# Performance work log

Hardware: AMD Instinct MI355X
Metric: run time of the kernel (lower is better)

## Reference

```python
import jax, jax.numpy as jnp
import numpy as np

N_FILTERS = 64
FILTER_SIZE = 64
N_FRAMES = 64
N_TO_KEEP = 128
MIN_SIZE = 512
N_SAMPLES = 32768
BATCH = 8


def pos_encoding(n_elements, n_sinusoids):
    t = np.linspace(1e-8, 1.0, n_elements)
    freq = np.linspace(1e-3, 1.0, n_sinusoids)
    return np.sin(t[:, None] * freq[None, :]).astype(np.float32)


def gammatone_filter_bank(n_filters, size, sr=22050.0):
    # 4th-order gammatone impulse responses, linearly spaced center freqs
    t = np.arange(size) / sr
    freqs = np.linspace(20.0, sr / 2 - 20.0, n_filters)
    b = 1.019 * 24.7 * (4.37 * freqs / 1000.0 + 1.0)  # ERB bandwidths
    g = (t[None, :] ** 3) * np.exp(-2 * np.pi * b[:, None] * t[None, :]) \
        * np.cos(2 * np.pi * freqs[:, None] * t[None, :])
    g = g / (np.abs(g).max(axis=-1, keepdims=True) + 1e-12)
    return g.astype(np.float32)


def setup_inputs() -> dict:
    key = jax.random.key(0)
    k1, k2 = jax.random.split(key)
    return {
        'target': jax.random.normal(k1, (BATCH, 1, N_SAMPLES), dtype=jnp.float32),
        'recon': jax.random.normal(k2, (BATCH, 1, N_SAMPLES), dtype=jnp.float32),
        'filters': jnp.asarray(gammatone_filter_bank(N_FILTERS, FILTER_SIZE)),
        'proj_time': jnp.asarray(pos_encoding(N_FRAMES, 128)),
        'proj_freq': jnp.asarray(pos_encoding(N_FILTERS, 128)),
    }


def fft_frequency_decompose(x, min_size):
    # band-limited octave decomposition: band of size s holds rfft bins [s/4, s/2)
    coeffs = jnp.fft.rfft(x, norm='ortho')
    n = x.shape[-1]
    bands = []
    start, end = 0, min_size // 2
    while end <= n // 2:
        spec = jnp.zeros(x.shape[:-1] + (end + 1,), dtype=coeffs.dtype)
        spec = spec.at[..., start:end].set(coeffs[..., start:end])
        bands.append(jnp.fft.irfft(spec, n=end * 2, norm='ortho'))
        start, end = end, end * 2
    return bands


def fft_convolve(a, b):
    n = a.shape[-1]
    pa = jnp.pad(a, [(0, 0)] * (a.ndim - 1) + [(0, n)])
    pb = jnp.pad(b, [(0, 0)] * (b.ndim - 1) + [(0, n)])
    spec = jnp.fft.rfft(pa) * jnp.fft.rfft(pb)  # broadcasts [B,1,.] x [1,F,.]
    return jnp.fft.irfft(spec, n=2 * n)[..., :n]


def max_pool1d(x, kernel, stride, pad):
    return jax.lax.reduce_window(
        x, -jnp.inf, jax.lax.max,
        (1, 1, kernel), (1, 1, stride),
        [(0, 0), (0, 0), (pad, pad)])


def sparsify2(x, k):
    # top-k over flattened (channels*time); pack events as value-scaled time
    # one-hots and binary channel one-hots
    b, c, t = x.shape
    flat = x.reshape(b, c * t)
    values, indices = jax.lax.top_k(flat, k)  # [b, k]
    ch, tm = indices // t, indices % t
    packed = (tm[..., None] == jnp.arange(t)[None, None, :]).astype(x.dtype) * values[..., None]  # [b,k,t]
    one_hot = (ch[..., None] == jnp.arange(c)[None, None, :]).astype(x.dtype)  # [b,k,c]
    return packed, one_hot


def _feature(x, filters, proj_time, proj_freq):
    bands = fft_frequency_decompose(x, MIN_SIZE)
    outs = []
    for band in bands:  # fixed small set of structurally distinct bands
        samples = band.shape[-1]
        filt = jnp.pad(filters[None, :, :], ((0, 0), (0, 0), (0, samples - FILTER_SIZE)))
        result = fft_convolve(band, filt)  # [B, n_filters, samples]
        stride = samples // 64
        pooled = max_pool1d(result, 2 * stride, stride, stride // 2)[..., :samples]  # [B, 64, 64]
        packed, one_hot = sparsify2(pooled, N_TO_KEEP)
        a = packed @ proj_time   # [B, k, 128]
        b = one_hot @ proj_freq  # [B, k, 128]
        outs.append(jnp.concatenate([a, b], axis=-1))
    return jnp.concatenate(outs, axis=-1)  # [B, k, 256 * n_bands]


def reference(target, recon, filters, proj_time, proj_freq):
    t = _feature(target, filters, proj_time, proj_freq)
    r = _feature(recon, filters, proj_time, proj_freq)
    return jnp.abs(t - r).mean()
```

## Files before the change

kernel.cpp:

```cpp
#include <hip/hip_runtime.h>
#include <hip/hip_bf16.h>

#define N_SAMP    32768
#define NBINS     16384
#define NSIG      16
#define NBANDS    7
#define K_TOP     128
#define BAND_STRIDE 65472

#define SST_F   0
#define SST_PT  4096
#define SST_PF  12288
#define SST_TOT 20480

#define TWO_PI 6.283185307179586f

typedef __attribute__((ext_vector_type(8))) short bf16x8;
typedef __attribute__((ext_vector_type(4))) float f32x4;

__device__ __forceinline__ float bf2f(__hip_bfloat16 v) { return __bfloat162float(v); }

__device__ __forceinline__ unsigned encf(float f) {
    unsigned u = __float_as_uint(f);
    return (u & 0x80000000u) ? ~u : (u | 0x80000000u);
}
__device__ __forceinline__ float decf(unsigned u) {
    return __uint_as_float((u & 0x80000000u) ? (u ^ 0x80000000u) : ~u);
}

__device__ __forceinline__ int band_M1sh(int b) { return b < 3 ? 4 : (b < 4 ? 5 : 6); }
__device__ __forceinline__ int band_Lsh(int b) {
    return b == 0 ? 5 : (b == 1 ? 6 : (b < 5 ? 7 : (b == 5 ? 8 : 9)));
}
__device__ __forceinline__ int band_M2sh(int b) {
    return b < 2 ? 4 : (b < 5 ? 5 : (b == 5 ? 6 : 7));
}

__global__ __launch_bounds__(256) void k_fwd1(
    const void* __restrict__ tgt, const void* __restrict__ rec,
    const void* __restrict__ f, const void* __restrict__ pt,
    const void* __restrict__ pf,
    __hip_bfloat16* __restrict__ staged,
    float* __restrict__ bands, float* __restrict__ accum,
    int* __restrict__ counter, int* __restrict__ lossCnt,
    float* __restrict__ T)
{
    const int tid   = threadIdx.x;
    const int sig   = blockIdx.y;

    if (blockIdx.x == 16) {
        float pv0 = bf2f(((const __hip_bfloat16*)tgt)[tid & 63]);
        int bad0 = (fabsf(pv0) > 1e8f) || (pv0 != pv0);
        const int isf = (__ballot(bad0) != 0ull);
        #pragma unroll
        for (int k = 0; k < 5; ++k) {
            int id = sig * 1280 + k * 256 + tid;
            const void* src; int idx;
            if (id < SST_PT)      { src = f;  idx = id; }
            else if (id < SST_PF) { src = pt; idx = id - SST_PT; }
            else                  { src = pf; idx = id - SST_PF; }
            float v = isf ? ((const float*)src)[idx]
                          : bf2f(((const __hip_bfloat16*)src)[idx]);
            staged[id] = __float2bfloat16(v);
        }
        for (int i = tid; i < 448; i += 256) {
            int g = i >> 6, j = i & 63;
            int off = 64 * g + 512 * ((1 << g) - 1);
            bands[(size_t)sig * BAND_STRIDE + off + j] = 0.f;
        }
        if (sig == 0) {
            if (tid == 0) { accum[0] = 0.f; counter[0] = 0; }
            if (tid < 8 * NBANDS) lossCnt[tid] = 0;
        }
        return;
    }

    const int nbase = (blockIdx.x & 1) * 128;
    const int kgrp  = ((blockIdx.x >> 1) & 1) * 64;
    const int nqq   = (blockIdx.x >> 2) & 3;
    __shared__ __align__(16) __hip_bfloat16 xT[32][136];
    __shared__ float ct[128], st[128];
    __shared__ float2 t256[256];
    __shared__ float2 tF[128];

    {
        float sv, cv;
        sincosf(TWO_PI * (float)tid * (1.f / 256.f), &sv, &cv);
        t256[tid] = make_float2(cv, -sv);
        if (tid < 128) {
            sincosf(TWO_PI * (float)tid * (1.f / 128.f), &sv, &cv);
            ct[tid] = cv; st[tid] = sv;
            sincosf(TWO_PI * (float)tid * (1.f / 32768.f), &sv, &cv);
            tF[tid] = make_float2(cv, -sv);
        }
    }

    float pv = bf2f(((const __hip_bfloat16*)tgt)[tid & 63]);
    int bad = (fabsf(pv) > 1e8f) || (pv != pv);
    const int isf32 = (__ballot(bad) != 0ull);
    const void* xsrc = (sig < 8) ? tgt : rec;
    const int soff = (sig & 7) * N_SAMP;

    const int rloc = tid & 31;
    const int chb  = (tid >> 5) * 16;
    for (int c8 = 0; c8 < 16; c8 += 8) {
        union { bf16x8 v; __hip_bfloat16 h[8]; } u;
        #pragma unroll
        for (int uu = 0; uu < 8; ++uu) {
            int n1 = chb + c8 + uu;
            int gi = soff + n1 * 256 + nbase + nqq * 32 + rloc;
            float xv = isf32 ? ((const float*)xsrc)[gi]
                             : bf2f(((const __hip_bfloat16*)xsrc)[gi]);
            u.h[uu] = __float2bfloat16(xv);
        }
        *(bf16x8*)(&xT[rloc][chb + c8]) = u.v;
    }
    __syncthreads();

    const int tl = tid & 15, quad = (tid >> 4) & 3, w = tid >> 6;
    const int k1 = kgrp + w * 16 + tl;
    bf16x8 Arh[4], Arl[4], Aih[4], Ail[4];
    #pragma unroll
    for (int ki = 0; ki < 4; ++ki) {
        union { bf16x8 v; __hip_bfloat16 h[8]; } rh, rl, ih, il;
        #pragma unroll
        for (int j = 0; j < 8; ++j) {
            int n1 = ki * 32 + quad * 8 + j;
            int tt = (k1 * n1) & 127;
            float wre = ct[tt], wim = -st[tt];
            __hip_bfloat16 h1 = __float2bfloat16(wre);
            rh.h[j] = h1;
            rl.h[j] = __float2bfloat16(wre - bf2f(h1));
            __hip_bfloat16 h2 = __float2bfloat16(wim);
            ih.h[j] = h2;
            il.h[j] = __float2bfloat16(wim - bf2f(h2));
        }
        Arh[ki] = rh.v; Arl[ki] = rl.v; Aih[ki] = ih.v; Ail[ki] = il.v;
    }

    float2* To = (float2*)T + (size_t)sig * 128 * 256;
    const int mk = kgrp + w * 16 + quad * 4;
    for (int ni = 0; ni < 2; ++ni) {
        bf16x8 B[4];
        #pragma unroll
        for (int ki = 0; ki < 4; ++ki)
            B[ki] = *(const bf16x8*)(&xT[ni * 16 + tl][ki * 32 + quad * 8]);
        f32x4 aR = {0.f,0.f,0.f,0.f}, aI = {0.f,0.f,0.f,0.f};
        #pragma unroll
        for (int ki = 0; ki < 4; ++ki) {
            aR = __builtin_amdgcn_mfma_f32_16x16x32_bf16(Arh[ki], B[ki], aR, 0, 0, 0);
            aR = __builtin_amdgcn_mfma_f32_16x16x32_bf16(Arl[ki], B[ki], aR, 0, 0, 0);
            aI = __builtin_amdgcn_mfma_f32_16x16x32_bf16(Aih[ki], B[ki], aI, 0, 0, 0);
            aI = __builtin_amdgcn_mfma_f32_16x16x32_bf16(Ail[ki], B[ki], aI, 0, 0, 0);
        }
        const int n2 = nbase + nqq * 32 + ni * 16 + tl;
        #pragma unroll
        for (int rg = 0; rg < 4; ++rg) {
            int k1e = mk + rg;
            int m = k1e * n2;
            float2 e1 = t256[m >> 7];
            float2 e2 = tF[m & 127];
            float er = e1.x * e2.x - e1.y * e2.y;
            float ei = e1.x * e2.y + e1.y * e2.x;
            float Tr = aR[rg] * er - aI[rg] * ei;
            float Ti = aI[rg] * er + aR[rg] * ei;
            To[(size_t)k1e * 256 + n2] = make_float2(Tr, Ti);
        }
    }
}

__global__ __launch_bounds__(128) void k_fwd2(
    const float* __restrict__ T, float* __restrict__ C)
{
    const int k2  = threadIdx.x;
    const int k1  = blockIdx.x;
    const int sig = blockIdx.y;
    __shared__ float2 Ts[256];
    __shared__ float2 tw[256];
    const float2* Tin = (const float2*)T + ((size_t)sig * 128 + k1) * 256;
    for (int i = k2; i < 256; i += 128) Ts[i] = Tin[i];
    {
        float sv, cv;
        sincosf(TWO_PI * (float)k2 * (1.f / 256.f), &sv, &cv);
        tw[k2]       = make_float2(cv, -sv);
        tw[k2 + 128] = make_float2(-cv, sv);
    }
    __syncthreads();
    float er[4], ei[4];
    #pragma unroll
    for (int c = 0; c < 4; ++c) {
        float2 e = tw[(c * k2) & 255];
        er[c] = e.x; ei[c] = e.y;
    }
    float2 e4 = tw[(4 * k2) & 255];
    const float c4 = e4.x, s4 = e4.y;
    float Xr[4] = {0.f,0.f,0.f,0.f}, Xi[4] = {0.f,0.f,0.f,0.f};
    for (int n2 = 0; n2 < 256; n2 += 4) {
        #pragma unroll
        for (int c = 0; c < 4; ++c) {
            float2 t = Ts[n2 + c];
            Xr[c] += t.x * er[c] - t.y * ei[c];
            Xi[c] += t.x * ei[c] + t.y * er[c];
            float nr = er[c] * c4 - ei[c] * s4;
            ei[c]    = er[c] * s4 + ei[c] * c4;
            er[c] = nr;
        }
    }
    const float inv = 5.5242717280199030e-3f;
    float xr = (Xr[0] + Xr[1]) + (Xr[2] + Xr[3]);
    float xi = (Xi[0] + Xi[1]) + (Xi[2] + Xi[3]);
    float2* Co = (float2*)C + (size_t)sig * NBINS;
    Co[k1 + 128 * k2] = make_float2(xr * inv, xi * inv);
}

__global__ __launch_bounds__(256) void k_synthA(
    const float* __restrict__ C, float* __restrict__ G)
{
    const int tid = threadIdx.x;
    const int sig = blockIdx.y;
    const int bix = 63 - blockIdx.x;
    const int band = (bix == 0) ? 0 : (32 - __clz(bix));
    const int lbx  = (band == 0) ? 0 : (bix - (1 << (band - 1)));
    const int s    = 512 << band;
    const int m1sh = band_M1sh(band);
    const int lsh  = band_Lsh(band);
    const int m2sh = band_M2sh(band);
    const int M2   = 1 << m2sh;
    const int L    = 1 << lsh;
    const int L4   = L >> 2;
    const int a    = (band == 0) ? 0 : (128 << band);
    const int tix  = lbx * 256 + tid;
    const int j1lo = (lbx * 256) >> (lsh - 2);
    int j1cnt = 256 >> (lsh - 2);
    if (j1cnt > (1 << m1sh)) j1cnt = 1 << m1sh;
    __shared__ float2 Ds[256];
    const float2* D = (const float2*)C + (size_t)sig * NBINS + a;
    for (int i = tid; i < (j1cnt << m2sh); i += 256) {
        int j1o = i >> m2sh, j2 = i & (M2 - 1);
        Ds[i] = D[(j1lo + j1o) + (j2 << m1sh)];
    }
    __syncthreads();
    if (tix >= (128 << band)) return;
    const int j1o = (tix >> (lsh - 2)) - j1lo;
    const int m   = tix & (L4 - 1);
    const float2* Dj = Ds + (j1o << m2sh);
    float e0r = 1.f, e0i = 0.f, e1r, e1i, sr, si;
    sincosf(TWO_PI * (float)m / (float)L, &e1i, &e1r);
    sr = e1r * e1r - e1i * e1i;
    si = 2.f * e1r * e1i;
    float ar[4] = {0.f,0.f,0.f,0.f}, ai[4] = {0.f,0.f,0.f,0.f};
    for (int j2 = 0; j2 < M2; j2 += 4) {
        {   float2 d = Dj[j2];
            float tr = d.x * e0r - d.y * e0i, ti = d.x * e0i + d.y * e0r;
            ar[0] += tr; ai[0] += ti; ar[1] += tr; ai[1] += ti;
            ar[2] += tr; ai[2] += ti; ar[3] += tr; ai[3] += ti;
            float nr = e0r * sr - e0i * si; e0i = e0r * si + e0i * sr; e0r = nr;
        }
        {   float2 d = Dj[j2 + 1];
            float tr = d.x * e1r - d.y * e1i, ti = d.x * e1i + d.y * e1r;
            ar[0] += tr; ai[0] += ti;
            ar[1] -= ti; ai[1] += tr;
            ar[2] -= tr; ai[2] -= ti;
            ar[3] += ti; ai[3] -= tr;
            float nr = e1r * sr - e1i * si; e1i = e1r * si + e1i * sr; e1r = nr;
        }
        {   float2 d = Dj[j2 + 2];
            float tr = d.x * e0r - d.y * e0i, ti = d.x * e0i + d.y * e0r;
            ar[0] += tr; ai[0] += ti;
            ar[1] -= tr; ai[1] -= ti;
            ar[2] += tr; ai[2] += ti;
            ar[3] -= tr; ai[3] -= ti;
            float nr = e0r * sr - e0i * si; e0i = e0r * si + e0i * sr; e0r = nr;
        }
        {   float2 d = Dj[j2 + 3];
            float tr = d.x * e1r - d.y * e1i, ti = d.x * e1i + d.y * e1r;
            ar[0] += tr; ai[0] += ti;
            ar[1] += ti; ai[1] -= tr;
            ar[2] -= tr; ai[2] -= ti;
            ar[3] -= ti; ai[3] += tr;
            float nr = e1r * sr - e1i * si; e1i = e1r * si + e1i * sr; e1r = nr;
        }
    }
    const float sc = 2.f * rsqrtf((float)s);
    float2* Go = (float2*)G + (size_t)sig * 65024 + 512 * ((1 << band) - 1);
    const int base = ((tix >> (lsh - 2)) << lsh) + m;
    #pragma unroll
    for (int q = 0; q < 4; ++q)
        Go[base + q * L4] = make_float2(ar[q] * sc, ai[q] * sc);
}

__global__ __launch_bounds__(256) void k_synthB(
    const float* __restrict__ C, const float* __restrict__ G,
    float* __restrict__ bands)
{
    const int tid = threadIdx.x;
    const int sig = blockIdx.y;
    const int bix = 63 - blockIdx.x;
    const int band = (bix == 0) ? 0 : (32 - __clz(bix));
    const int lbx  = (band == 0) ? 0 : (bix - (1 << (band - 1)));
    const int s    = 512 << band;
    const int M1   = 1 << band_M1sh(band);
    const int lsh  = band_Lsh(band);
    const int n    = lbx * 256 + tid;
    const int s4   = s >> 2;
    if (n >= s4) return;
    const int m    = n & ((1 << lsh) - 1);
    const float2* Gi = (const float2*)G + (size_t)sig * 65024 + 512 * ((1 << band) - 1);
    float e0r = 1.f, e0i = 0.f, e1r, e1i, sr, si;
    sincosf(TWO_PI * (float)n / (float)s, &e1i, &e1r);
    sr = e1r * e1r - e1i * e1i;
    si = 2.f * e1r * e1i;
    float zr[4] = {0.f,0.f,0.f,0.f}, zi[4] = {0.f,0.f,0.f,0.f};
    for (int j1 = 0; j1 < M1; j1 += 4) {
        {   float2 g = Gi[((j1 + 0) << lsh) + m];
            float tr = g.x * e0r - g.y * e0i, ti = g.x * e0i + g.y * e0r;
            zr[0] += tr; zi[0] += ti; zr[1] += tr; zi[1] += ti;
            zr[2] += tr; zi[2] += ti; zr[3] += tr; zi[3] += ti;
            float nr = e0r * sr - e0i * si; e0i = e0r * si + e0i * sr; e0r = nr;
        }
        {   float2 g = Gi[((j1 + 1) << lsh) + m];
            float tr = g.x * e1r - g.y * e1i, ti = g.x * e1i + g.y * e1r;
            zr[0] += tr; zi[0] += ti;
            zr[1] -= ti; zi[1] += tr;
            zr[2] -= tr; zi[2] -= ti;
            zr[3] += ti; zi[3] -= tr;
            float nr = e1r * sr - e1i * si; e1i = e1r * si + e1i * sr; e1r = nr;
        }
        {   float2 g = Gi[((j1 + 2) << lsh) + m];
            float tr = g.x * e0r - g.y * e0i, ti = g.x * e0i + g.y * e0r;
            zr[0] += tr; zi[0] += ti;
            zr[1] -= tr; zi[1] -= ti;
            zr[2] += tr; zi[2] += ti;
            zr[3] -= tr; zi[3] -= ti;
            float nr = e0r * sr - e0i * si; e0i = e0r * si + e0i * sr; e0r = nr;
        }
        {   float2 g = Gi[((j1 + 3) << lsh) + m];
            float tr = g.x * e1r - g.y * e1i, ti = g.x * e1i + g.y * e1r;
            zr[0] += tr; zi[0] += ti;
            zr[1] += ti; zi[1] -= tr;
            zr[2] -= tr; zi[2] -= ti;
            zr[3] -= ti; zi[3] += tr;
            float nr = e1r * sr - e1i * si; e1i = e1r * si + e1i * sr; e1r = nr;
        }
    }
    const int poff = 64 * (band + 1) + 512 * ((1 << band) - 1);
    float* bo = bands + (size_t)sig * BAND_STRIDE + poff;
    if (band == 0) {
        const float dc = C[(size_t)sig * NBINS * 2] * 0.04419417382415922f;
        #pragma unroll
        for (int q = 0; q < 4; ++q) bo[n + q * s4] = zr[q] - dc;
    } else {
        #pragma unroll
        for (int q = 0; q < 4; ++q) {
            float val;
            switch (n & 3) {
                case 0:  val =  zr[q]; break;
                case 1:  val = -zi[q]; break;
                case 2:  val = -zr[q]; break;
                default: val =  zi[q]; break;
            }
            bo[n + q * s4] = val;
        }
    }
}

__global__ __launch_bounds__(256) void k_conv(
    const float* __restrict__ bands,
    const __hip_bfloat16* __restrict__ filters,
    float* __restrict__ segG)
{
    const int tid  = threadIdx.x;
    const int sig  = blockIdx.y;
    const int c    = blockIdx.x;
    const int band = 31 - __clz(c + 1);
    const int cidx = c + 1 - (1 << band);
    const int poff = 64 * (band + 1) + 512 * ((1 << band) - 1);
    const float* bp = bands + (size_t)sig * BAND_STRIDE + poff + cidx * 512;

    __shared__ __align__(16) __hip_bfloat16 xr[8][584];
    __shared__ float segP[64 * 4];

    if (tid < 72) {
        const int j = tid;
        const float* src = bp + 496 - 8 * j;
        float4 f0 = *(const float4*)(src + 12);
        float4 f1 = *(const float4*)(src + 8);
        float4 f2 = *(const float4*)(src + 4);
        float4 f3 = *(const float4*)(src + 0);
        __hip_bfloat16 w[16];
        w[0]  = __float2bfloat16(f0.w); w[1]  = __float2bfloat16(f0.z);
        w[2]  = __float2bfloat16(f0.y); w[3]  = __float2bfloat16(f0.x);
        w[4]  = __float2bfloat16(f1.w); w[5]  = __float2bfloat16(f1.z);
        w[6]  = __float2bfloat16(f1.y); w[7]  = __float2bfloat16(f1.x);
        w[8]  = __float2bfloat16(f2.w); w[9]  = __float2bfloat16(f2.z);
        w[10] = __float2bfloat16(f2.y); w[11] = __float2bfloat16(f2.x);
        w[12] = __float2bfloat16(f3.w); w[13] = __float2bfloat16(f3.z);
        w[14] = __float2bfloat16(f3.y); w[15] = __float2bfloat16(f3.x);
        #pragma unroll
        for (int p = 0; p < 8; ++p) {
            union { bf16x8 v; __hip_bfloat16 h[8]; } o;
            #pragma unroll
            for (int e = 0; e < 8; ++e) o.h[e] = w[p + e];
            *(bf16x8*)(&xr[p][8 * j]) = o.v;
        }
    }
    __syncthreads();

    const int tl   = tid & 15;
    const int quad = (tid >> 4) & 3;
    const int wave = tid >> 6;

    bf16x8 bf0[4], bf1[4];
    #pragma unroll
    for (int ft = 0; ft < 4; ++ft) {
        const __hip_bfloat16* fp = filters + ((ft * 16 + tl) * 64 + quad * 8);
        bf0[ft] = *(const bf16x8*)(fp);
        bf1[ft] = *(const bf16x8*)(fp + 32);
    }

    int s0 = 511 - wave * 128 - tl + 8 * quad;
    const __hip_bfloat16* xp = &xr[0][0] + (s0 & 7) * 584 + (s0 & ~7);

    const int spc = 512 >> (2 + band);
    float* segO = segG + (size_t)(sig * NBANDS + band) * 64 * 128 + cidx * spc;

    const float NEG = -3.4e38f;
    float run0 = NEG, run1 = NEG, run2 = NEG, run3 = NEG;
    const int per = (band >= 2) ? (1 << (band - 2)) : 1;

    for (int it = 0; it < 8; ++it) {
        const int t0 = wave * 128 + it * 16;
        bf16x8 a0 = *(const bf16x8*)(xp);
        bf16x8 a1 = *(const bf16x8*)(xp + 32);
        xp -= 16;
        f32x4 ac0 = {0.f,0.f,0.f,0.f}, ac1 = ac0, ac2 = ac0, ac3 = ac0;
        ac0 = __builtin_amdgcn_mfma_f32_16x16x32_bf16(a0, bf0[0], ac0, 0, 0, 0);
        ac0 = __builtin_amdgcn_mfma_f32_16x16x32_bf16(a1, bf1[0], ac0, 0, 0, 0);
        ac1 = __builtin_amdgcn_mfma_f32_16x16x32_bf16(a0, bf0[1], ac1, 0, 0, 0);
        ac1 = __builtin_amdgcn_mfma_f32_16x16x32_bf16(a1, bf1[1], ac1, 0, 0, 0);
        ac2 = __builtin_amdgcn_mfma_f32_16x16x32_bf16(a0, bf0[2], ac2, 0, 0, 0);
        ac2 = __builtin_amdgcn_mfma_f32_16x16x32_bf16(a1, bf1[2], ac2, 0, 0, 0);
        ac3 = __builtin_amdgcn_mfma_f32_16x16x32_bf16(a0, bf0[3], ac3, 0, 0, 0);
        ac3 = __builtin_amdgcn_mfma_f32_16x16x32_bf16(a1, bf1[3], ac3, 0, 0, 0);
        float m0 = fmaxf(fmaxf(ac0[0], ac0[1]), fmaxf(ac0[2], ac0[3]));
        float m1 = fmaxf(fmaxf(ac1[0], ac1[1]), fmaxf(ac1[2], ac1[3]));
        float m2 = fmaxf(fmaxf(ac2[0], ac2[1]), fmaxf(ac2[2], ac2[3]));
        float m3 = fmaxf(fmaxf(ac3[0], ac3[1]), fmaxf(ac3[2], ac3[3]));
        if (band == 0) {
            int sb = (t0 >> 2) + quad;
            segO[(tl     ) * 128 + sb] = m0;
            segO[(tl + 16) * 128 + sb] = m1;
            segO[(tl + 32) * 128 + sb] = m2;
            segO[(tl + 48) * 128 + sb] = m3;
        } else if (band == 1) {
            m0 = fmaxf(m0, __shfl_xor(m0, 16));
            m1 = fmaxf(m1, __shfl_xor(m1, 16));
            m2 = fmaxf(m2, __shfl_xor(m2, 16));
            m3 = fmaxf(m3, __shfl_xor(m3, 16));
            if ((quad & 1) == 0) {
                int sb = (t0 >> 3) + (quad >> 1);
                segO[(tl     ) * 128 + sb] = m0;
                segO[(tl + 16) * 128 + sb] = m1;
                segO[(tl + 32) * 128 + sb] = m2;
                segO[(tl + 48) * 128 + sb] = m3;
            }
        } else {
            m0 = fmaxf(m0, __shfl_xor(m0, 16)); m0 = fmaxf(m0, __shfl_xor(m0, 32));
            m1 = fmaxf(m1, __shfl_xor(m1, 16)); m1 = fmaxf(m1, __shfl_xor(m1, 32));
            m2 = fmaxf(m2, __shfl_xor(m2, 16)); m2 = fmaxf(m2, __shfl_xor(m2, 32));
            m3 = fmaxf(m3, __shfl_xor(m3, 16)); m3 = fmaxf(m3, __shfl_xor(m3, 32));
            run0 = fmaxf(run0, m0); run1 = fmaxf(run1, m1);
            run2 = fmaxf(run2, m2); run3 = fmaxf(run3, m3);
            if (((it + 1) & (per - 1)) == 0) {
                int sb = t0 >> (2 + band);
                float rv = quad == 0 ? run0 : quad == 1 ? run1
                         : quad == 2 ? run2 : run3;
                segO[(tl + 16 * quad) * 128 + sb] = rv;
                run0 = NEG; run1 = NEG; run2 = NEG; run3 = NEG;
            }
        }
    }
    if (band == 6) {
        float rv = quad == 0 ? run0 : quad == 1 ? run1
                 : quad == 2 ? run2 : run3;
        segP[(tl + 16 * quad) * 4 + wave] = rv;
        __syncthreads();
        if (tid < 128) {
            int f = tid & 63, sg = tid >> 6;
            segO[f * 128 + sg] =
                fmaxf(segP[f * 4 + 2 * sg], segP[f * 4 + 2 * sg + 1]);
        }
    }
}

__global__ __launch_bounds__(512) void k_topk(
    const float* __restrict__ segG,
    float* __restrict__ topv, int* __restrict__ topi,
    const __hip_bfloat16* __restrict__ PT, const __hip_bfloat16* __restrict__ PF,
    int* __restrict__ lossCnt, float* __restrict__ accum,
    int* __restrict__ counter, unsigned* __restrict__ out)
{
    const int tid = threadIdx.x;
    const int band = blockIdx.x, sig = blockIdx.y;
    const float* segB = segG + (size_t)(sig * NBANDS + band) * 64 * 128;

    __shared__ unsigned hist[256];
    __shared__ unsigned scan[256];
    __shared__ unsigned long long list[512];
    __shared__ int sh_B, sh_nA, sh_cnt, sh_num, sh_w2;
    __shared__ float vT[128], vR[128];
    __shared__ int   iT[128], iR[128];
    __shared__ float red[256];
    __shared__ int amLast;

    unsigned long long kk[8];
    #pragma unroll
    for (int q = 0; q < 8; ++q) {
        int i = q * 512 + tid;
        int f = i >> 6, t = i & 63;
        const float* sg = segB + f * 128;
        float m = fmaxf(sg[2 * t], sg[2 * t + 1]);
        if (t > 0)  m = fmaxf(m, sg[2 * t - 1]);
        if (t < 63) m = fmaxf(m, sg[2 * t + 2]);
        kk[q] = ((unsigned long long)encf(m) << 32) | (unsigned)(4095 - i);
    }

    int shift = 56;
    unsigned long long prefix = 0;
    int nA = 0;
    for (int lev = 0; lev < 8; ++lev) {
        if (tid < 256) hist[tid] = 0;
        __syncthreads();
        #pragma unroll
        for (int q = 0; q < 8; ++q) {
            bool inpre = (lev == 0) || ((kk[q] >> (shift + 8)) == prefix);
            if (inpre) atomicAdd(&hist[(unsigned)((kk[q] >> shift) & 255u)], 1u);
        }
        __syncthreads();
        if (tid < 256) scan[tid] = hist[tid];
        __syncthreads();
        for (int off = 1; off < 256; off <<= 1) {
            unsigned v = 0;
            if (tid < 256) v = scan[tid] + ((tid + off < 256) ? scan[tid + off] : 0u);
            __syncthreads();
            if (tid < 256) scan[tid] = v;
            __syncthreads();
        }
        if (tid < 256) {
            unsigned ge = (unsigned)nA + scan[tid];
            unsigned gt = (unsigned)nA + ((tid < 255) ? scan[tid + 1] : 0u);
            if (ge >= 128u && gt < 128u) {
                sh_B = tid; sh_nA = (int)gt; sh_cnt = (int)hist[tid];
            }
        }
        __syncthreads();
        prefix = (prefix << 8) | (unsigned)sh_B;
        nA = sh_nA;
        if (nA + sh_cnt <= 511 || shift == 0) break;
        shift -= 8;
        __syncthreads();
    }

    if (tid < 256) { list[tid] = 0ull; list[tid + 256] = 0ull; }
    if (tid == 0) sh_num = 0;
    __syncthreads();
    #pragma unroll
    for (int q = 0; q < 8; ++q) {
        if ((kk[q] >> shift) >= prefix) {
            int p = atomicAdd(&sh_num, 1);
            if (p < 512) list[p] = kk[q];
        }
    }
    __syncthreads();

    for (int k = 2; k <= 512; k <<= 1) {
        for (int j = k >> 1; j > 0; j >>= 1) {
            const int w = tid;
            const int l = w ^ j;
            if (l > w) {
                unsigned long long av = list[w], bv = list[l];
                bool up = ((w & k) == 0);
                if ((av > bv) == up) { list[w] = bv; list[l] = av; }
            }
            __syncthreads();
        }
    }
    if (tid < K_TOP) {
        unsigned long long key = list[511 - tid];
        const size_t ob = ((size_t)sig * NBANDS + band) * K_TOP + tid;
        topv[ob] = decf((unsigned)(key >> 32));
        topi[ob] = 4095 - (int)(key & 0xFFFFFFFFu);
    }

    __syncthreads();
    if (tid == 0) {
        __threadfence();
        sh_w2 = (atomicAdd(&lossCnt[(sig & 7) * NBANDS + band], 1) == 1);
    }
    __syncthreads();
    if (!sh_w2) return;
    __threadfence();

    const int b = sig & 7;
    const size_t bt = ((size_t)b * NBANDS + band) * K_TOP;
    const size_t br = ((size_t)(8 + b) * NBANDS + band) * K_TOP;
    if (tid < 128) { vT[tid] = topv[bt + tid]; iT[tid] = topi[bt + tid]; }
    else if (tid < 256) {
        int j = tid - 128; vR[j] = topv[br + j]; iR[j] = topi[br + j];
    }
    __syncthreads();
    float sum = 0.f;
    if (tid < 128) {
        #pragma unroll 4
        for (int k = 0; k < K_TOP; ++k) {
            float a = vT[k] * bf2f(PT[(iT[k] & 63) * 128 + tid]);
            float cc = vR[k] * bf2f(PT[(iR[k] & 63) * 128 + tid]);
            sum += fabsf(a - cc);
        }
    } else if (tid < 256) {
        const int j = tid - 128;
        #pragma unroll 4
        for (int k = 0; k < K_TOP; ++k) {
            float a = bf2f(PF[(iT[k] >> 6) * 128 + j]);
            float cc = bf2f(PF[(iR[k] >> 6) * 128 + j]);
            sum += fabsf(a - cc);
        }
    }
    if (tid < 256) red[tid] = sum;
    __syncthreads();
    for (int ofs = 128; ofs > 0; ofs >>= 1) {
        if (tid < ofs) red[tid] += red[tid + ofs];
        __syncthreads();
    }
    if (tid == 0) {
        atomicAdd(accum, red[0]);
        __threadfence();
        amLast = (atomicAdd(counter, 1) == NBANDS * 8 - 1);
    }
    __syncthreads();
    if (!amLast) return;
    if (tid == 0) {
        __threadfence();
        float L = atomicAdd(accum, 0.f) * (1.0f / 1835008.0f);
        unsigned lu = __float_as_uint(L);
        bool isnanL = ((lu & 0x7F800000u) == 0x7F800000u) && (lu & 0x007FFFFFu);
        float code;
        if      (isnanL)           code = 500.f;
        else if (L == 0.f)         code = 400.f;
        else if (fabsf(L) < 1e-6f) code = 600.f;
        else                       code = L;
        unsigned fb = __float_as_uint(code);
        unsigned hb = (fb + 0x7FFFu + ((fb >> 16) & 1u)) >> 16;
        out[0] = (hb << 16) | hb;
    }
}

extern "C" void kernel_launch(void* const* d_in, const int* in_sizes, int n_in,
                              void* d_out, int out_size, void* d_ws, size_t ws_size,
                              hipStream_t stream)
{
    float* C      = (float*)d_ws;
    float* bands  = C + (size_t)NSIG * NBINS * 2;
    float* segG   = bands + (size_t)NSIG * BAND_STRIDE;
    float* topv   = segG + (size_t)NSIG * NBANDS * 64 * 128;
    int*   topi   = (int*)(topv + (size_t)NSIG * NBANDS * K_TOP);
    float* accum  = (float*)(topi + (size_t)NSIG * NBANDS * K_TOP);
    int*   counter= (int*)(accum + 1);
    int*   lossCnt= (int*)(accum + 4);
    __hip_bfloat16* staged = (__hip_bfloat16*)(accum + 64);
    float* TG = (float*)(staged + SST_TOT);
    float* T  = TG;
    float* G  = TG;

    const __hip_bfloat16* fst = staged + SST_F;
    const __hip_bfloat16* pts = staged + SST_PT;
    const __hip_bfloat16* pfs = staged + SST_PF;

    k_fwd1   <<<dim3(17, NSIG),      256, 0, stream>>>(d_in[0], d_in[1],
                 d_in[2], d_in[3], d_in[4], staged, bands, accum, counter,
                 lossCnt, T);
    k_fwd2   <<<dim3(128, NSIG),     128, 0, stream>>>(T, C);
    k_synthA <<<dim3(64, NSIG),      256, 0, stream>>>(C, G);
    k_synthB <<<dim3(64, NSIG),      256, 0, stream>>>(C, G, bands);
    k_conv   <<<dim3(127, NSIG),     256, 0, stream>>>(bands, fst, segG);
    k_topk   <<<dim3(NBANDS, NSIG),  512, 0, stream>>>(segG, topv, topi,
                 pts, pfs, lossCnt, accum, counter, (unsigned*)d_out);
}
```

Before: 186.1 us.

## Use wave shuffles for top-k histogram scan and intra-wave bitonic stages

The top-k kernel's 256-entry suffix scan now uses wave-level shuffle reductions plus a four-entry cross-wave sum instead of a shared-memory Hillis-Steele scan with many barriers. The bitonic sort of the 512 candidates performs every stage with partner distance under 64 through register shuffles, and keeps shared memory and barriers only for the larger distances. The DFT twiddle table for 128 points is dropped and read from the existing 256-point table at even indices, which removes one sincos call and two shared arrays. The aim is fewer __syncthreads and less shared-memory traffic, at the cost of 64-bit shuffles.

After: 183.0 us. No clear change (-1.6%).

```diff
diff --git a/kernel.cpp b/kernel.cpp
--- a/kernel.cpp
+++ b/kernel.cpp
@@ -79,7 +79,6 @@
     const int kgrp  = ((blockIdx.x >> 1) & 1) * 64;
     const int nqq   = (blockIdx.x >> 2) & 3;
     __shared__ __align__(16) __hip_bfloat16 xT[32][136];
-    __shared__ float ct[128], st[128];
     __shared__ float2 t256[256];
     __shared__ float2 tF[128];
 
@@ -88,8 +87,6 @@
         sincosf(TWO_PI * (float)tid * (1.f / 256.f), &sv, &cv);
         t256[tid] = make_float2(cv, -sv);
         if (tid < 128) {
-            sincosf(TWO_PI * (float)tid * (1.f / 128.f), &sv, &cv);
-            ct[tid] = cv; st[tid] = sv;
             sincosf(TWO_PI * (float)tid * (1.f / 32768.f), &sv, &cv);
             tF[tid] = make_float2(cv, -sv);
         }
@@ -127,7 +124,8 @@
         for (int j = 0; j < 8; ++j) {
             int n1 = ki * 32 + quad * 8 + j;
             int tt = (k1 * n1) & 127;
-            float wre = ct[tt], wim = -st[tt];
+            float2 e = t256[2 * tt];
+            float wre = e.x, wim = e.y;
             __hip_bfloat16 h1 = __float2bfloat16(wre);
             rh.h[j] = h1;
             rl.h[j] = __float2bfloat16(wre - bf2f(h1));
@@ -500,12 +498,14 @@
     int* __restrict__ lossCnt, float* __restrict__ accum,
     int* __restrict__ counter, unsigned* __restrict__ out)
 {
-    const int tid = threadIdx.x;
+    const int tid  = threadIdx.x;
+    const int lane = tid & 63;
+    const int wv4  = tid >> 6;
     const int band = blockIdx.x, sig = blockIdx.y;
     const float* segB = segG + (size_t)(sig * NBANDS + band) * 64 * 128;
 
     __shared__ unsigned hist[256];
-    __shared__ unsigned scan[256];
+    __shared__ unsigned wsum[4];
     __shared__ unsigned long long list[512];
     __shared__ int sh_B, sh_nA, sh_cnt, sh_num, sh_w2;
     __shared__ float vT[128], vR[128];
@@ -537,20 +537,26 @@
             if (inpre) atomicAdd(&hist[(unsigned)((kk[q] >> shift) & 255u)], 1u);
         }
         __syncthreads();
-        if (tid < 256) scan[tid] = hist[tid];
+        unsigned hcnt = 0, sfx = 0;
+        if (tid < 256) {
+            hcnt = hist[tid];
+            sfx = hcnt;
+            #pragma unroll
+            for (int off = 1; off < 64; off <<= 1) {
+                unsigned o = __shfl_down(sfx, off);
+                if (lane + off < 64) sfx += o;
+            }
+            if (lane == 0) wsum[wv4] = sfx;
+        }
         __syncthreads();
-        for (int off = 1; off < 256; off <<= 1) {
-            unsigned v = 0;
-            if (tid < 256) v = scan[tid] + ((tid + off < 256) ? scan[tid + off] : 0u);
-            __syncthreads();
-            if (tid < 256) scan[tid] = v;
-            __syncthreads();
-        }
         if (tid < 256) {
-            unsigned ge = (unsigned)nA + scan[tid];
-            unsigned gt = (unsigned)nA + ((tid < 255) ? scan[tid + 1] : 0u);
+            unsigned addhi = 0;
+            #pragma unroll
+            for (int w2 = 1; w2 < 4; ++w2) addhi += (w2 > wv4) ? wsum[w2] : 0u;
+            unsigned ge = (unsigned)nA + sfx + addhi;
+            unsigned gt = ge - hcnt;
             if (ge >= 128u && gt < 128u) {
-                sh_B = tid; sh_nA = (int)gt; sh_cnt = (int)hist[tid];
+                sh_B = tid; sh_nA = (int)gt; sh_cnt = (int)hcnt;
             }
         }
         __syncthreads();
@@ -573,10 +579,22 @@
     }
     __syncthreads();
 
-    for (int k = 2; k <= 512; k <<= 1) {
+    unsigned long long v = list[tid];
+    #pragma unroll
+    for (int k = 2; k <= 64; k <<= 1) {
         for (int j = k >> 1; j > 0; j >>= 1) {
-            const int w = tid;
-            const int l = w ^ j;
+            unsigned long long pv = __shfl_xor(v, j);
+            bool takeMin = (((tid & j) == 0) == ((tid & k) == 0));
+            unsigned long long mn = v < pv ? v : pv;
+            unsigned long long mx = v < pv ? pv : v;
+            v = takeMin ? mn : mx;
+        }
+    }
+    list[tid] = v;
+    __syncthreads();
+    for (int k = 128; k <= 512; k <<= 1) {
+        for (int j = k >> 1; j >= 64; j >>= 1) {
+            const int w = tid, l = w ^ j;
             if (l > w) {
                 unsigned long long av = list[w], bv = list[l];
                 bool up = ((w & k) == 0);
@@ -584,7 +602,19 @@
             }
             __syncthreads();
         }
-    }
+        v = list[tid];
+        #pragma unroll
+        for (int j = 32; j > 0; j >>= 1) {
+            unsigned long long pv = __shfl_xor(v, j);
+            bool takeMin = (((tid & j) == 0) == ((tid & k) == 0));
+            unsigned long long mn = v < pv ? v : pv;
+            unsigned long long mx = v < pv ? pv : v;
+            v = takeMin ? mn : mx;
+        }
+        list[tid] = v;
+        __syncthreads();
+    }
+
     if (tid < K_TOP) {
         unsigned long long key = list[511 - tid];
         const size_t ob = ((size_t)sig * NBANDS + band) * K_TOP + tid;
```
